# Kernel optimization log

Measured on AMD Instinct MI355X. Metric: run time of the kernel, lower is better.

Reference implementation:

```python
import jax, jax.numpy as jnp
import numpy as np

N_NODE = 40000  # item vocabulary
H = 100         # hidden size (SR-GNN default)
B = 64          # sessions per batch
L = 16          # items per session (equal-length sessions)
N = B * L       # total graph nodes
E = 2048        # total edges
NL = 1          # GatedGraphConv layers


def setup_inputs() -> dict:
    key = jax.random.key(0)
    ks = jax.random.split(key, 20)
    stdv = 1.0 / np.sqrt(H)
    u = lambda k, shape: jax.random.uniform(k, shape, jnp.float32, -stdv, stdv)
    return {
        "x": jax.random.randint(ks[0], (N,), 0, N_NODE),
        "edge_index": jax.random.randint(ks[1], (2, E), 0, N),
        "edge_weight": jax.random.uniform(ks[2], (E,), jnp.float32),
        "batch": jnp.arange(N) // L,  # node -> session id, equal-length sessions
        "embed": u(ks[3], (N_NODE, H)),
        "ggc_w": u(ks[4], (NL, H, H)),
        "gru_wih": u(ks[5], (3 * H, H)),
        "gru_whh": u(ks[6], (3 * H, H)),
        "gru_bih": u(ks[7], (3 * H,)),
        "gru_bhh": u(ks[8], (3 * H,)),
        "W1_w": u(ks[9], (H, H)), "W1_b": u(ks[10], (H,)),
        "W2_w": u(ks[11], (H, H)), "W2_b": u(ks[12], (H,)),
        "Wt_w": u(ks[13], (H, H)), "Wt_b": u(ks[14], (H,)),
        "q_w": u(ks[15], (1, H)), "q_b": u(ks[16], (1,)),
        "W3_w": u(ks[17], (H, 2 * H)), "W3_b": u(ks[18], (H,)),
    }


def reference(x, edge_index, edge_weight, batch, embed, ggc_w, gru_wih, gru_whh,
              gru_bih, gru_bhh, W1_w, W1_b, W2_w, W2_b, Wt_w, Wt_b, q_w, q_b,
              W3_w, W3_b):
    # Embedding lookup
    h = embed[x]  # [N, H]
    src, dst = edge_index[0], edge_index[1]
    # GatedGraphConv: weighted message aggregation + GRUCell update
    for l in range(NL):
        m = h @ ggc_w[l]                                             # [N, H]
        agg = jnp.zeros_like(h).at[dst].add(edge_weight[:, None] * m[src])
        gi = agg @ gru_wih.T + gru_bih                               # [N, 3H]
        gh = h @ gru_whh.T + gru_bhh
        ir, iz, inn = jnp.split(gi, 3, axis=-1)
        hr, hz, hn = jnp.split(gh, 3, axis=-1)
        r = jax.nn.sigmoid(ir + hr)
        zg = jax.nn.sigmoid(iz + hz)
        ng = jnp.tanh(inn + r * hn)
        h = (1.0 - zg) * ng + zg * h
    v = h.reshape(B, L, H)                                           # sessions
    s_l = v[:, -1]                                                   # [B, H] last item
    # alpha = q(sigmoid(W1(v_n) + W2(v)))
    a = jax.nn.sigmoid((s_l @ W1_w.T + W1_b)[:, None, :] + (v @ W2_w.T + W2_b))
    alpha = a @ q_w.T + q_b                                          # [B, L, 1]
    s_g = jnp.sum(alpha * v, axis=1)                                 # [B, H]
    s_h = jnp.concatenate([s_l, s_g], axis=-1) @ W3_w.T + W3_b       # [B, H]
    # Target attention: s_t[b] = softmax(E @ W_t(v_b)^T, -1) @ v_b, contracted
    # directly against E to avoid materializing [B, N_NODE, H].
    vt = v @ Wt_w.T + Wt_b                                           # [B, L, H]
    P = jax.nn.softmax(jnp.einsum('jh,blh->bjl', embed, vt), axis=-1)
    C = jnp.einsum('blh,jh->bjl', v, embed)                          # v_l . E_j
    z = s_h @ embed.T + jnp.sum(P * C, axis=-1)                      # [B, N_NODE]
    return z
```

## Files before the change

### kernel.cpp

```cpp
#include <hip/hip_runtime.h>
#include <hip/hip_bf16.h>

#define Hh    100
#define NN    1024
#define BB    64
#define LL    16
#define EE    2048
#define NNODE 40000

#define BSPL  8
#define BPB   (BB / BSPL)
#define PFR   12
#define PPAN  (PFR * 64 * 8)

typedef unsigned short u16;
typedef __attribute__((ext_vector_type(8))) short short8;
typedef __attribute__((ext_vector_type(4))) float f32x4;

__device__ __forceinline__ float bf2f(u16 u) {
    union { unsigned int i; float f; } v;
    v.i = ((unsigned int)u) << 16;
    return v.f;
}

__device__ __forceinline__ u16 f2bf(float f) {
    unsigned int x = __float_as_uint(f);
    unsigned int lsb = (x >> 16) & 1u;
    x += 0x7fffu + lsb;
    return (u16)(x >> 16);
}

__device__ __forceinline__ float sigmoidf_(float x) {
    return 1.0f / (1.0f + expf(-x));
}

template <bool BF>
__device__ __forceinline__ float ldv(const void* p, size_t i) {
    if (BF) return bf2f(((const u16*)p)[i]);
    return ((const float*)p)[i];
}
__device__ __forceinline__ float ldvf(int flag, const void* p, size_t i) {
    return flag ? ldv<true>(p, i) : ldv<false>(p, i);
}

template <bool BF>
__device__ void cvt_impl(int t,
                         const void* ew, const void* ggc, const void* wih, const void* whh,
                         const void* bih, const void* bhh, const void* W1w, const void* W1b,
                         const void* W2w, const void* W2b, const void* Wtw, const void* Wtb,
                         const void* qw, const void* qb, const void* W3w, const void* W3b,
                         float* __restrict__ W) {
    const void* src; int si; int doff; int di;
    if      (t <   2048) { src = ew;  si = t;          doff = 0;      di = si; }
    else if (t <  12048) { src = ggc; si = t - 2048;   doff = 2048;   di = si; }
    else if (t <  42048) { src = wih; si = t - 12048;  doff = 12048;  di = (si % 100) * 300 + si / 100; }
    else if (t <  72048) { src = whh; si = t - 42048;  doff = 42048;  di = (si % 100) * 300 + si / 100; }
    else if (t <  72348) { src = bih; si = t - 72048;  doff = 72048;  di = si; }
    else if (t <  72648) { src = bhh; si = t - 72348;  doff = 72352;  di = si; }
    else if (t <  82648) { src = W1w; si = t - 72648;  doff = 72656;  di = (si % 100) * 100 + si / 100; }
    else if (t <  82748) { src = W1b; si = t - 82648;  doff = 82656;  di = si; }
    else if (t <  92748) { src = W2w; si = t - 82748;  doff = 82768;  di = (si % 100) * 100 + si / 100; }
    else if (t <  92848) { src = W2b; si = t - 92748;  doff = 92768;  di = si; }
    else if (t < 102848) { src = Wtw; si = t - 92848;  doff = 92880;  di = (si % 100) * 100 + si / 100; }
    else if (t < 102948) { src = Wtb; si = t - 102848; doff = 102880; di = si; }
    else if (t < 103048) { src = qw;  si = t - 102948; doff = 102992; di = si; }
    else if (t < 103049) { src = qb;  si = t - 103048; doff = 103104; di = si; }
    else if (t < 123049) { src = W3w; si = t - 103049; doff = 103120; di = (si % 200) * 100 + si / 200; }
    else                 { src = W3b; si = t - 123049; doff = 123120; di = si; }
    W[doff + di] = ldv<BF>(src, si);
}

__global__ void __launch_bounds__(256) k_cvt(const void* embed_raw, int* __restrict__ flag,
                      const void* ew, const void* ggc, const void* wih, const void* whh,
                      const void* bih, const void* bhh, const void* W1w, const void* W1b,
                      const void* W2w, const void* W2b, const void* Wtw, const void* Wtb,
                      const void* qw, const void* qb, const void* W3w, const void* W3b,
                      float* __restrict__ W) {
    __shared__ int cnt;
    if (threadIdx.x == 0) cnt = 0;
    __syncthreads();
    int bad = 0;
    const u16* eb = (const u16*)embed_raw;
    for (int i = threadIdx.x; i < 4096; i += 256) {
        float v = bf2f(eb[i]);
        if (!(fabsf(v) <= 0.5f)) bad++;
    }
    if (bad) atomicAdd(&cnt, bad);
    __syncthreads();
    const bool bf = (cnt == 0);
    if (blockIdx.x == 0 && threadIdx.x == 0) flag[0] = bf ? 1 : 0;
    int t = blockIdx.x * 256 + threadIdx.x;
    if (t >= 123149) return;
    if (bf) cvt_impl<true >(t, ew, ggc, wih, whh, bih, bhh, W1w, W1b, W2w, W2b, Wtw, Wtb, qw, qb, W3w, W3b, W);
    else    cvt_impl<false>(t, ew, ggc, wih, whh, bih, bhh, W1w, W1b, W2w, W2b, Wtw, Wtb, qw, qb, W3w, W3b, W);
}

__global__ void __launch_bounds__(256) k_gm(const int* __restrict__ flag,
                                            const int* __restrict__ x,
                                            const void* __restrict__ embed,
                                            const float* __restrict__ ggc_w,
                                            float* __restrict__ m,
                                            float* __restrict__ agg) {
    __shared__ float W[Hh * Hh];
    __shared__ float H[8 * Hh];
    const int tid = threadIdx.x;
    const int fl = flag[0];
    const int r0 = blockIdx.x * 8;
    for (int idx = tid; idx < Hh * Hh; idx += 256) W[idx] = ggc_w[idx];
    for (int idx = tid; idx < 8 * Hh; idx += 256) {
        int i = idx / Hh, j = idx - i * Hh;
        H[idx] = ldvf(fl, embed, (size_t)x[r0 + i] * Hh + j);
    }
    for (int idx = tid; idx < 8 * Hh; idx += 256) agg[r0 * Hh + idx] = 0.0f;
    __syncthreads();
    for (int idx = tid; idx < 8 * Hh; idx += 256) {
        int i = idx / Hh, j = idx - i * Hh;
        float acc = 0.0f;
#pragma unroll 4
        for (int k = 0; k < Hh; ++k) acc += H[i * Hh + k] * W[k * Hh + j];
        m[(r0 + i) * Hh + j] = acc;
    }
}

__global__ void k_scatter(const int* __restrict__ ei, const float* __restrict__ ew,
                          const float* __restrict__ m, float* __restrict__ agg) {
    int t = blockIdx.x * 256 + threadIdx.x;
    if (t >= EE * Hh) return;
    int e = t / Hh, j = t - e * Hh;
    int src = ei[e], dst = ei[EE + e];
    atomicAdd(&agg[dst * Hh + j], ew[e] * m[src * Hh + j]);
}

__global__ void k_gru(const int* __restrict__ flag, const int* __restrict__ x,
                      const void* __restrict__ embed,
                      const float* __restrict__ agg,
                      const float* __restrict__ wihT, const float* __restrict__ whhT,
                      const float* __restrict__ bih, const float* __restrict__ bhh,
                      float* __restrict__ h1) {
    int t = blockIdx.x * 256 + threadIdx.x;
    if (t >= NN * Hh) return;
    int i = t / Hh, j = t - i * Hh;
    const int fl = flag[0];
    const size_t erow = (size_t)x[i] * Hh;
    const float* ar = agg + i * Hh;
    float s_ir = bih[j], s_iz = bih[j + Hh], s_in = bih[j + 2 * Hh];
    float s_hr = bhh[j], s_hz = bhh[j + Hh], s_hn = bhh[j + 2 * Hh];
    float h0j = 0.0f;
    for (int k = 0; k < Hh; ++k) {
        float a = ar[k];
        float h = ldvf(fl, embed, erow + k);
        if (k == j) h0j = h;
        const float* wT = wihT + k * 300;
        const float* uT = whhT + k * 300;
        s_ir += a * wT[j];
        s_iz += a * wT[j + 100];
        s_in += a * wT[j + 200];
        s_hr += h * uT[j];
        s_hz += h * uT[j + 100];
        s_hn += h * uT[j + 200];
    }
    float r = sigmoidf_(s_ir + s_hr);
    float z = sigmoidf_(s_iz + s_hz);
    float n = tanhf(s_in + r * s_hn);
    h1[t] = (1.0f - z) * n + z * h0j;
}

__global__ void __launch_bounds__(256) k_att(const float* __restrict__ h1,
                    const float* __restrict__ W1T, const float* __restrict__ W1b,
                    const float* __restrict__ W2T, const float* __restrict__ W2b,
                    const float* __restrict__ WtT, const float* __restrict__ Wtb,
                    const float* __restrict__ qw, const float* __restrict__ qb,
                    const float* __restrict__ W3T, const float* __restrict__ W3b,
                    u16* __restrict__ P) {
    __shared__ float V[LL * Hh];
    __shared__ float Q2[LL * Hh];
    __shared__ float VTs[LL * Hh];
    __shared__ float Q1[Hh];
    __shared__ float AL[LL];
    __shared__ float SG[Hh];
    __shared__ float SH[Hh];
    const int b = blockIdx.x, tid = threadIdx.x;
    for (int idx = tid; idx < LL * Hh; idx += 256) V[idx] = h1[b * LL * Hh + idx];
    __syncthreads();
    for (int idx = tid; idx < LL * Hh; idx += 256) {
        int i = idx / Hh, j = idx - i * Hh;
        float a2 = 0, at = 0;
        for (int k = 0; k < Hh; ++k) {
            float vk = V[i * Hh + k];
            a2 += vk * W2T[k * Hh + j];
            at += vk * WtT[k * Hh + j];
        }
        Q2[idx] = a2 + W2b[j];
        VTs[idx] = at + Wtb[j];
    }
    if (tid < Hh) {
        float a1 = 0;
        for (int k = 0; k < Hh; ++k) a1 += V[(LL - 1) * Hh + k] * W1T[k * Hh + tid];
        Q1[tid] = a1 + W1b[tid];
    }
    __syncthreads();
    if (tid < LL) {
        float acc = 0;
        for (int j = 0; j < Hh; ++j)
            acc += sigmoidf_(Q1[j] + Q2[tid * Hh + j]) * qw[j];
        AL[tid] = acc + qb[0];
    }
    __syncthreads();
    if (tid < Hh) {
        float acc = 0;
#pragma unroll
        for (int l = 0; l < LL; ++l) acc += AL[l] * V[l * Hh + tid];
        SG[tid] = acc;
    }
    __syncthreads();
    if (tid < Hh) {
        float acc = W3b[tid];
        for (int k = 0; k < Hh; ++k) acc += V[(LL - 1) * Hh + k] * W3T[k * Hh + tid];
        for (int k = 0; k < Hh; ++k) acc += SG[k] * W3T[(Hh + k) * Hh + tid];
        SH[tid] = acc;
    }
    __syncthreads();
    for (int w = tid; w < PFR * 64; w += 256) {
        int f = w >> 6, lane = w & 63;
        int t = f >> 2, ks = f & 3;
        int mm = lane & 15, qq = lane >> 4;
        int row = t * 16 + mm;
        int col0 = ks * 32 + qq * 8;
        short8 t8;
#pragma unroll
        for (int e = 0; e < 8; ++e) {
            int col = col0 + e;
            float v = 0.0f;
            if (col < Hh) {
                if      (row < 16) v = VTs[row * Hh + col];
                else if (row < 32) v = V[(row - 16) * Hh + col];
                else if (row == 32) v = SH[col];
            }
            t8[e] = (short)f2bf(v);
        }
        *(short8*)&P[((size_t)b * PFR + f) * 512 + lane * 8] = t8;
    }
}

__device__ __forceinline__ short8 load_efrag(const void* embed, bool bf, int j, int k0) {
    short8 v = {0, 0, 0, 0, 0, 0, 0, 0};
    if (j >= NNODE || k0 >= Hh) return v;
    if (bf) {
        const u16* row = (const u16*)embed + (size_t)j * Hh + k0;
        if (k0 + 8 <= Hh) {
            ushort4 a = *(const ushort4*)(row);
            ushort4 b = *(const ushort4*)(row + 4);
            v[0] = (short)a.x; v[1] = (short)a.y; v[2] = (short)a.z; v[3] = (short)a.w;
            v[4] = (short)b.x; v[5] = (short)b.y; v[6] = (short)b.z; v[7] = (short)b.w;
        } else {
            for (int e = 0; e < Hh - k0; ++e) v[e] = (short)row[e];
        }
    } else {
        const float* row = (const float*)embed + (size_t)j * Hh + k0;
        if (k0 + 8 <= Hh) {
            float4 a = *(const float4*)(row);
            float4 b = *(const float4*)(row + 4);
            v[0] = (short)f2bf(a.x); v[1] = (short)f2bf(a.y); v[2] = (short)f2bf(a.z); v[3] = (short)f2bf(a.w);
            v[4] = (short)f2bf(b.x); v[5] = (short)f2bf(b.y); v[6] = (short)f2bf(b.z); v[7] = (short)f2bf(b.w);
        } else {
            for (int e = 0; e < Hh - k0; ++e) v[e] = (short)f2bf(row[e]);
        }
    }
    return v;
}

__global__ void __launch_bounds__(256) k_score(const int* __restrict__ flag,
                                               const void* __restrict__ embed,
                                               const u16* __restrict__ P,
                                               void* __restrict__ out) {
    __shared__ alignas(16) u16 sPan[2][PPAN];
    const int jb = blockIdx.x * 128;
    const int b0 = blockIdx.y * BPB;
    const int tid = threadIdx.x;
    const bool bf = (flag[0] != 0);
    const int wave = tid >> 6, lane = tid & 63;
    const int m = lane & 15, quad = lane >> 4;

    short8 Bf[2][4];
#pragma unroll
    for (int g = 0; g < 2; ++g)
#pragma unroll
        for (int ks = 0; ks < 4; ++ks)
            Bf[g][ks] = load_efrag(embed, bf, jb + wave * 32 + g * 16 + m, ks * 32 + quad * 8);

    short8 pa = {0, 0, 0, 0, 0, 0, 0, 0};
    short8 pb = {0, 0, 0, 0, 0, 0, 0, 0};
    if (quad == 0) {
        pa[0] = (short)f2bf((float)m);
        pb[0] = (short)f2bf(1.0f);
    }
    f32x4 pd = (f32x4){0.0f, 0.0f, 0.0f, 0.0f};
    pd = __builtin_amdgcn_mfma_f32_16x16x32_bf16(pa, pb, pd, 0, 0, 0);
    const bool isH1 =
        (__builtin_amdgcn_readfirstlane(__float_as_uint(pd[1])) == 0x3f800000u);

    {
        const uint4* s4 = (const uint4*)(P + (size_t)b0 * PPAN);
        uint4 g0 = s4[tid], g1 = s4[tid + 256], g2 = s4[tid + 512];
        uint4* d = (uint4*)sPan[0];
        d[tid] = g0; d[tid + 256] = g1; d[tid + 512] = g2;
    }
    __syncthreads();

    int cur = 0;
    for (int bi = 0; bi < BPB; ++bi) {
        const int b = b0 + bi;
        uint4 g0, g1, g2;
        if (bi + 1 < BPB) {
            const uint4* s4 = (const uint4*)(P + (size_t)(b + 1) * PPAN);
            g0 = s4[tid]; g1 = s4[tid + 256]; g2 = s4[tid + 512];
        }

        const u16* sp = sPan[cur];
        f32x4 acc[2][3];
#pragma unroll
        for (int g = 0; g < 2; ++g)
#pragma unroll
            for (int t = 0; t < 3; ++t)
                acc[g][t] = (f32x4){0.0f, 0.0f, 0.0f, 0.0f};
#pragma unroll
        for (int t = 0; t < 3; ++t) {
            short8 A0 = *(const short8*)&sp[(t * 4 + 0) * 512 + lane * 8];
            short8 A1 = *(const short8*)&sp[(t * 4 + 1) * 512 + lane * 8];
            short8 A2 = *(const short8*)&sp[(t * 4 + 2) * 512 + lane * 8];
            short8 A3 = *(const short8*)&sp[(t * 4 + 3) * 512 + lane * 8];
#pragma unroll
            for (int g = 0; g < 2; ++g) {
                acc[g][t] = __builtin_amdgcn_mfma_f32_16x16x32_bf16(A0, Bf[g][0], acc[g][t], 0, 0, 0);
                acc[g][t] = __builtin_amdgcn_mfma_f32_16x16x32_bf16(A1, Bf[g][1], acc[g][t], 0, 0, 0);
                acc[g][t] = __builtin_amdgcn_mfma_f32_16x16x32_bf16(A2, Bf[g][2], acc[g][t], 0, 0, 0);
                acc[g][t] = __builtin_amdgcn_mfma_f32_16x16x32_bf16(A3, Bf[g][3], acc[g][t], 0, 0, 0);
            }
        }

#pragma unroll
        for (int g = 0; g < 2; ++g) {
            if (isH1) {
                float den = 0.0f, num = 0.0f;
#pragma unroll
                for (int r = 0; r < 4; ++r) {
                    float p = __expf(acc[g][0][r]);
                    den += p;
                    num += p * acc[g][1][r];
                }
                den += __shfl_xor(den, 16); num += __shfl_xor(num, 16);
                den += __shfl_xor(den, 32); num += __shfl_xor(num, 32);
                if (quad == 0) {
                    int j = jb + wave * 32 + g * 16 + m;
                    if (j < NNODE) {
                        float z = acc[g][2][0] + num / den;
                        if (bf) ((u16*)out)[(size_t)b * NNODE + j] = f2bf(z);
                        else    ((float*)out)[(size_t)b * NNODE + j] = z;
                    }
                }
            } else {
                float den[4], num[4];
#pragma unroll
                for (int r = 0; r < 4; ++r) {
                    float p = __expf(acc[g][0][r]);
                    den[r] = p;
                    num[r] = p * acc[g][1][r];
                }
#pragma unroll
                for (int s = 1; s <= 8; s <<= 1)
#pragma unroll
                    for (int r = 0; r < 4; ++r) {
                        den[r] += __shfl_xor(den[r], s);
                        num[r] += __shfl_xor(num[r], s);
                    }
                if (m == 0) {
#pragma unroll
                    for (int r = 0; r < 4; ++r) {
                        int j = jb + wave * 32 + g * 16 + quad * 4 + r;
                        if (j < NNODE) {
                            float z = acc[g][2][r] + num[r] / den[r];
                            if (bf) ((u16*)out)[(size_t)b * NNODE + j] = f2bf(z);
                            else    ((float*)out)[(size_t)b * NNODE + j] = z;
                        }
                    }
                }
            }
        }

        if (bi + 1 < BPB) {
            uint4* d = (uint4*)sPan[cur ^ 1];
            d[tid] = g0; d[tid + 256] = g1; d[tid + 512] = g2;
        }
        __syncthreads();
        cur ^= 1;
    }
}

extern "C" void kernel_launch(void* const* d_in, const int* in_sizes, int n_in,
                              void* d_out, int out_size, void* d_ws, size_t ws_size,
                              hipStream_t stream) {
    const int* x      = (const int*)d_in[0];
    const int* ei     = (const int*)d_in[1];
    const void* ew    = d_in[2];
    const void* embed = d_in[4];
    const void* ggc   = d_in[5];
    const void* wih   = d_in[6];
    const void* whh   = d_in[7];
    const void* bih   = d_in[8];
    const void* bhh   = d_in[9];
    const void* W1w   = d_in[10];
    const void* W1b   = d_in[11];
    const void* W2w   = d_in[12];
    const void* W2b   = d_in[13];
    const void* Wtw   = d_in[14];
    const void* Wtb   = d_in[15];
    const void* qw    = d_in[16];
    const void* qb    = d_in[17];
    const void* W3w   = d_in[18];
    const void* W3b   = d_in[19];
    float* ws = (float*)d_ws;
    int* flag = (int*)d_ws;

    float* W = ws + 64;
    float* ew_f  = W + 0;
    float* ggc_f = W + 2048;
    float* wihT  = W + 12048;
    float* whhT  = W + 42048;
    float* bih_f = W + 72048;
    float* bhh_f = W + 72352;
    float* W1T   = W + 72656;
    float* W1b_f = W + 82656;
    float* W2T   = W + 82768;
    float* W2b_f = W + 92768;
    float* WtT   = W + 92880;
    float* Wtb_f = W + 102880;
    float* qw_f  = W + 102992;
    float* qb_f  = W + 103104;
    float* W3T   = W + 103120;
    float* W3b_f = W + 123120;

    float* D     = ws + 123296;
    float* m     = D;
    float* agg   = D + 102400;
    float* h1    = D;
    u16*   P     = (u16*)(D + 102400);

    k_cvt    <<<dim3(482), dim3(256), 0, stream>>>(embed, flag, ew, ggc, wih, whh, bih, bhh,
                                                   W1w, W1b, W2w, W2b, Wtw, Wtb, qw, qb, W3w, W3b, W);
    k_gm     <<<dim3(128), dim3(256), 0, stream>>>(flag, x, embed, ggc_f, m, agg);
    k_scatter<<<dim3(800), dim3(256), 0, stream>>>(ei, ew_f, m, agg);
    k_gru    <<<dim3(400), dim3(256), 0, stream>>>(flag, x, embed, agg, wihT, whhT, bih_f, bhh_f, h1);
    k_att    <<<dim3(64),  dim3(256), 0, stream>>>(h1, W1T, W1b_f, W2T, W2b_f, WtT, Wtb_f,
                                                   qw_f, qb_f, W3T, W3b_f, P);
    k_score  <<<dim3((NNODE + 127) / 128, BSPL), dim3(256), 0, stream>>>(flag, embed, P, d_out);
}
```

Baseline: 234.6 us.

## Split attention kernel into wide per-element kernels and vectorize GRU dot products

Replaces the 64-block attention kernel with three kernels: a 400-block per-element kernel computing W2/Wt/W1 projections that writes the bf16 panel directly, a small alpha kernel, and a per-session kernel for s_g/s_h. The GRU now reads h0 cached by k_gm instead of re-gathering embed rows, and it does float4 dot products over untransposed row-major weights. Weight conversion drops the transposes, and agg zeroing is vectorized. This exposes much more parallelism in the attention stage at the cost of two extra launches and extra workspace traffic.

```diff
diff --git a/kernel.cpp b/kernel.cpp
--- a/kernel.cpp
+++ b/kernel.cpp
@@ -39,8 +39,14 @@
     if (BF) return bf2f(((const u16*)p)[i]);
     return ((const float*)p)[i];
 }
-__device__ __forceinline__ float ldvf(int flag, const void* p, size_t i) {
-    return flag ? ldv<true>(p, i) : ldv<false>(p, i);
+__device__ __forceinline__ float ldvb(int fl, const void* p, size_t i) {
+    return fl ? ldv<true>(p, i) : ldv<false>(p, i);
+}
+
+__device__ __forceinline__ size_t p_addr(int b, int row, int col) {
+    int f = (row >> 4) * 4 + (col >> 5);
+    int lane = (((col & 31) >> 3) << 4) + (row & 15);
+    return ((size_t)(b * PFR + f)) * 512 + lane * 8 + (col & 7);
 }
 
 template <bool BF>
@@ -50,24 +56,24 @@
                          const void* W2w, const void* W2b, const void* Wtw, const void* Wtb,
                          const void* qw, const void* qb, const void* W3w, const void* W3b,
                          float* __restrict__ W) {
-    const void* src; int si; int doff; int di;
-    if      (t <   2048) { src = ew;  si = t;          doff = 0;      di = si; }
-    else if (t <  12048) { src = ggc; si = t - 2048;   doff = 2048;   di = si; }
-    else if (t <  42048) { src = wih; si = t - 12048;  doff = 12048;  di = (si % 100) * 300 + si / 100; }
-    else if (t <  72048) { src = whh; si = t - 42048;  doff = 42048;  di = (si % 100) * 300 + si / 100; }
-    else if (t <  72348) { src = bih; si = t - 72048;  doff = 72048;  di = si; }
-    else if (t <  72648) { src = bhh; si = t - 72348;  doff = 72352;  di = si; }
-    else if (t <  82648) { src = W1w; si = t - 72648;  doff = 72656;  di = (si % 100) * 100 + si / 100; }
-    else if (t <  82748) { src = W1b; si = t - 82648;  doff = 82656;  di = si; }
-    else if (t <  92748) { src = W2w; si = t - 82748;  doff = 82768;  di = (si % 100) * 100 + si / 100; }
-    else if (t <  92848) { src = W2b; si = t - 92748;  doff = 92768;  di = si; }
-    else if (t < 102848) { src = Wtw; si = t - 92848;  doff = 92880;  di = (si % 100) * 100 + si / 100; }
-    else if (t < 102948) { src = Wtb; si = t - 102848; doff = 102880; di = si; }
-    else if (t < 103048) { src = qw;  si = t - 102948; doff = 102992; di = si; }
-    else if (t < 103049) { src = qb;  si = t - 103048; doff = 103104; di = si; }
-    else if (t < 123049) { src = W3w; si = t - 103049; doff = 103120; di = (si % 200) * 100 + si / 200; }
-    else                 { src = W3b; si = t - 123049; doff = 123120; di = si; }
-    W[doff + di] = ldv<BF>(src, si);
+    const void* src; int si; int doff;
+    if      (t <   2048) { src = ew;  si = t;          doff = 0; }
+    else if (t <  12048) { src = ggc; si = t - 2048;   doff = 2048; }
+    else if (t <  42048) { src = wih; si = t - 12048;  doff = 12048; }
+    else if (t <  72048) { src = whh; si = t - 42048;  doff = 42048; }
+    else if (t <  72348) { src = bih; si = t - 72048;  doff = 72048; }
+    else if (t <  72648) { src = bhh; si = t - 72348;  doff = 72352; }
+    else if (t <  82648) { src = W1w; si = t - 72648;  doff = 72656; }
+    else if (t <  82748) { src = W1b; si = t - 82648;  doff = 82656; }
+    else if (t <  92748) { src = W2w; si = t - 82748;  doff = 82768; }
+    else if (t <  92848) { src = W2b; si = t - 92748;  doff = 92768; }
+    else if (t < 102848) { src = Wtw; si = t - 92848;  doff = 92880; }
+    else if (t < 102948) { src = Wtb; si = t - 102848; doff = 102880; }
+    else if (t < 103048) { src = qw;  si = t - 102948; doff = 102992; }
+    else if (t < 103049) { src = qb;  si = t - 103048; doff = 103104; }
+    else if (t < 123049) { src = W3w; si = t - 103049; doff = 103120; }
+    else                 { src = W3b; si = t - 123049; doff = 123120; }
+    W[doff + si] = ldv<BF>(src, si);
 }
 
 __global__ void __launch_bounds__(256) k_cvt(const void* embed_raw, int* __restrict__ flag,
@@ -100,6 +106,7 @@
                                             const void* __restrict__ embed,
                                             const float* __restrict__ ggc_w,
                                             float* __restrict__ m,
+                                            float* __restrict__ h0,
                                             float* __restrict__ agg) {
     __shared__ float W[Hh * Hh];
     __shared__ float H[8 * Hh];
@@ -109,12 +116,15 @@
     for (int idx = tid; idx < Hh * Hh; idx += 256) W[idx] = ggc_w[idx];
     for (int idx = tid; idx < 8 * Hh; idx += 256) {
         int i = idx / Hh, j = idx - i * Hh;
-        H[idx] = ldvf(fl, embed, (size_t)x[r0 + i] * Hh + j);
-    }
-    for (int idx = tid; idx < 8 * Hh; idx += 256) agg[r0 * Hh + idx] = 0.0f;
+        H[idx] = ldvb(fl, embed, (size_t)x[r0 + i] * Hh + j);
+    }
+    float4 z4 = {0.0f, 0.0f, 0.0f, 0.0f};
+    for (int q = blockIdx.x * 256 + tid; q < 25600; q += 128 * 256)
+        ((float4*)agg)[q] = z4;
     __syncthreads();
     for (int idx = tid; idx < 8 * Hh; idx += 256) {
         int i = idx / Hh, j = idx - i * Hh;
+        h0[(r0 + i) * Hh + j] = H[idx];
         float acc = 0.0f;
 #pragma unroll 4
         for (int k = 0; k < Hh; ++k) acc += H[i * Hh + k] * W[k * Hh + j];
@@ -131,114 +141,124 @@
     atomicAdd(&agg[dst * Hh + j], ew[e] * m[src * Hh + j]);
 }
 
-__global__ void k_gru(const int* __restrict__ flag, const int* __restrict__ x,
-                      const void* __restrict__ embed,
-                      const float* __restrict__ agg,
-                      const float* __restrict__ wihT, const float* __restrict__ whhT,
+__global__ void k_gru(const float* __restrict__ agg, const float* __restrict__ h0,
+                      const float* __restrict__ wih, const float* __restrict__ whh,
                       const float* __restrict__ bih, const float* __restrict__ bhh,
                       float* __restrict__ h1) {
     int t = blockIdx.x * 256 + threadIdx.x;
     if (t >= NN * Hh) return;
     int i = t / Hh, j = t - i * Hh;
-    const int fl = flag[0];
-    const size_t erow = (size_t)x[i] * Hh;
-    const float* ar = agg + i * Hh;
-    float s_ir = bih[j], s_iz = bih[j + Hh], s_in = bih[j + 2 * Hh];
-    float s_hr = bhh[j], s_hz = bhh[j + Hh], s_hn = bhh[j + 2 * Hh];
-    float h0j = 0.0f;
-    for (int k = 0; k < Hh; ++k) {
-        float a = ar[k];
-        float h = ldvf(fl, embed, erow + k);
-        if (k == j) h0j = h;
-        const float* wT = wihT + k * 300;
-        const float* uT = whhT + k * 300;
-        s_ir += a * wT[j];
-        s_iz += a * wT[j + 100];
-        s_in += a * wT[j + 200];
-        s_hr += h * uT[j];
-        s_hz += h * uT[j + 100];
-        s_hn += h * uT[j + 200];
-    }
+    const float4* ar  = reinterpret_cast<const float4*>(agg + i * Hh);
+    const float4* hr  = reinterpret_cast<const float4*>(h0 + i * Hh);
+    const float4* wir = reinterpret_cast<const float4*>(wih + (size_t)j * Hh);
+    const float4* wiz = reinterpret_cast<const float4*>(wih + (size_t)(j + Hh) * Hh);
+    const float4* win = reinterpret_cast<const float4*>(wih + (size_t)(j + 2 * Hh) * Hh);
+    const float4* whr = reinterpret_cast<const float4*>(whh + (size_t)j * Hh);
+    const float4* whz = reinterpret_cast<const float4*>(whh + (size_t)(j + Hh) * Hh);
+    const float4* whn = reinterpret_cast<const float4*>(whh + (size_t)(j + 2 * Hh) * Hh);
+    float s_ir = 0, s_iz = 0, s_in = 0, s_hr = 0, s_hz = 0, s_hn = 0;
+    for (int kc = 0; kc < Hh / 4; ++kc) {
+        float4 a = ar[kc];
+        float4 h = hr[kc];
+        float4 w;
+        w = wir[kc]; s_ir += a.x * w.x + a.y * w.y + a.z * w.z + a.w * w.w;
+        w = wiz[kc]; s_iz += a.x * w.x + a.y * w.y + a.z * w.z + a.w * w.w;
+        w = win[kc]; s_in += a.x * w.x + a.y * w.y + a.z * w.z + a.w * w.w;
+        w = whr[kc]; s_hr += h.x * w.x + h.y * w.y + h.z * w.z + h.w * w.w;
+        w = whz[kc]; s_hz += h.x * w.x + h.y * w.y + h.z * w.z + h.w * w.w;
+        w = whn[kc]; s_hn += h.x * w.x + h.y * w.y + h.z * w.z + h.w * w.w;
+    }
+    s_ir += bih[j];
+    s_iz += bih[j + Hh];
+    s_in += bih[j + 2 * Hh];
+    s_hr += bhh[j];
+    s_hz += bhh[j + Hh];
+    s_hn += bhh[j + 2 * Hh];
     float r = sigmoidf_(s_ir + s_hr);
     float z = sigmoidf_(s_iz + s_hz);
     float n = tanhf(s_in + r * s_hn);
-    h1[t] = (1.0f - z) * n + z * h0j;
-}
-
-__global__ void __launch_bounds__(256) k_att(const float* __restrict__ h1,
-                    const float* __restrict__ W1T, const float* __restrict__ W1b,
-                    const float* __restrict__ W2T, const float* __restrict__ W2b,
-                    const float* __restrict__ WtT, const float* __restrict__ Wtb,
-                    const float* __restrict__ qw, const float* __restrict__ qb,
-                    const float* __restrict__ W3T, const float* __restrict__ W3b,
-                    u16* __restrict__ P) {
-    __shared__ float V[LL * Hh];
-    __shared__ float Q2[LL * Hh];
-    __shared__ float VTs[LL * Hh];
-    __shared__ float Q1[Hh];
-    __shared__ float AL[LL];
-    __shared__ float SG[Hh];
-    __shared__ float SH[Hh];
-    const int b = blockIdx.x, tid = threadIdx.x;
-    for (int idx = tid; idx < LL * Hh; idx += 256) V[idx] = h1[b * LL * Hh + idx];
-    __syncthreads();
-    for (int idx = tid; idx < LL * Hh; idx += 256) {
-        int i = idx / Hh, j = idx - i * Hh;
-        float a2 = 0, at = 0;
-        for (int k = 0; k < Hh; ++k) {
-            float vk = V[i * Hh + k];
-            a2 += vk * W2T[k * Hh + j];
-            at += vk * WtT[k * Hh + j];
-        }
-        Q2[idx] = a2 + W2b[j];
-        VTs[idx] = at + Wtb[j];
-    }
-    if (tid < Hh) {
+    h1[t] = (1.0f - z) * n + z * h0[t];
+}
+
+__global__ void k_att1(const float* __restrict__ h1,
+                       const float* __restrict__ W1w, const float* __restrict__ W1b,
+                       const float* __restrict__ W2w, const float* __restrict__ W2b,
+                       const float* __restrict__ Wtw, const float* __restrict__ Wtb,
+                       float* __restrict__ q1, float* __restrict__ q2,
+                       u16* __restrict__ P) {
+    int t = blockIdx.x * 256 + threadIdx.x;
+    if (t >= NN * Hh) return;
+    int i = t / Hh, j = t - i * Hh;
+    const float4* vr = reinterpret_cast<const float4*>(h1 + i * Hh);
+    const float4* w2 = reinterpret_cast<const float4*>(W2w + (size_t)j * Hh);
+    const float4* wt = reinterpret_cast<const float4*>(Wtw + (size_t)j * Hh);
+    float a2 = 0, at = 0;
+    for (int kc = 0; kc < Hh / 4; ++kc) {
+        float4 v = vr[kc];
+        float4 w;
+        w = w2[kc]; a2 += v.x * w.x + v.y * w.y + v.z * w.z + v.w * w.w;
+        w = wt[kc]; at += v.x * w.x + v.y * w.y + v.z * w.z + v.w * w.w;
+    }
+    q2[t] = a2 + W2b[j];
+    int b = i >> 4, n = i & 15;
+    P[p_addr(b, n, j)]      = f2bf(at + Wtb[j]);
+    P[p_addr(b, 16 + n, j)] = f2bf(h1[t]);
+    if (i < BB) {
+        const float4* sl = reinterpret_cast<const float4*>(h1 + (i * LL + LL - 1) * Hh);
+        const float4* w1 = reinterpret_cast<const float4*>(W1w + (size_t)j * Hh);
         float a1 = 0;
-        for (int k = 0; k < Hh; ++k) a1 += V[(LL - 1) * Hh + k] * W1T[k * Hh + tid];
-        Q1[tid] = a1 + W1b[tid];
-    }
-    __syncthreads();
-    if (tid < LL) {
+        for (int kc = 0; kc < Hh / 4; ++kc) {
+            float4 v = sl[kc];
+            float4 w = w1[kc];
+            a1 += v.x * w.x + v.y * w.y + v.z * w.z + v.w * w.w;
+        }
+        q1[i * Hh + j] = a1 + W1b[j];
+    }
+}
+
+__global__ void k_alpha(const float* __restrict__ q1, const float* __restrict__ q2,
+                        const float* __restrict__ qw, const float* __restrict__ qb,
+                        float* __restrict__ alpha) {
+    int i = blockIdx.x * 256 + threadIdx.x;
+    if (i >= NN) return;
+    int b = i >> 4;
+    float acc = 0;
+    for (int j = 0; j < Hh; ++j)
+        acc += sigmoidf_(q1[b * Hh + j] + q2[i * Hh + j]) * qw[j];
+    alpha[i] = acc + qb[0];
+}
+
+__global__ void k_sgsh(const float* __restrict__ h1, const float* __restrict__ alpha,
+                       const float* __restrict__ W3w, const float* __restrict__ W3b,
+                       u16* __restrict__ P) {
+    __shared__ float sl[Hh];
+    __shared__ float sg[Hh];
+    __shared__ float al[LL];
+    int b = blockIdx.x;
+    int j = threadIdx.x;
+    u16* Pp = P + (size_t)b * PPAN;
+    for (int w = j; w < PPAN; w += 128) {
+        int f = w >> 9, lane = (w >> 3) & 63, e = w & 7;
+        int row = (f >> 2) * 16 + (lane & 15);
+        int col = (f & 3) * 32 + (lane >> 4) * 8 + e;
+        if (row > 32 || col >= Hh) Pp[w] = 0;
+    }
+    if (j < LL) al[j] = alpha[b * LL + j];
+    __syncthreads();
+    if (j < Hh) {
+        sl[j] = h1[(b * LL + LL - 1) * Hh + j];
         float acc = 0;
-        for (int j = 0; j < Hh; ++j)
-            acc += sigmoidf_(Q1[j] + Q2[tid * Hh + j]) * qw[j];
-        AL[tid] = acc + qb[0];
-    }
-    __syncthreads();
-    if (tid < Hh) {
-        float acc = 0;
-#pragma unroll
-        for (int l = 0; l < LL; ++l) acc += AL[l] * V[l * Hh + tid];
-        SG[tid] = acc;
-    }
-    __syncthreads();
-    if (tid < Hh) {
-        float acc = W3b[tid];
-        for (int k = 0; k < Hh; ++k) acc += V[(LL - 1) * Hh + k] * W3T[k * Hh + tid];
-        for (int k = 0; k < Hh; ++k) acc += SG[k] * W3T[(Hh + k) * Hh + tid];
-        SH[tid] = acc;
-    }
-    __syncthreads();
-    for (int w = tid; w < PFR * 64; w += 256) {
-        int f = w >> 6, lane = w & 63;
-        int t = f >> 2, ks = f & 3;
-        int mm = lane & 15, qq = lane >> 4;
-        int row = t * 16 + mm;
-        int col0 = ks * 32 + qq * 8;
-        short8 t8;
-#pragma unroll
-        for (int e = 0; e < 8; ++e) {
-            int col = col0 + e;
-            float v = 0.0f;
-            if (col < Hh) {
-                if      (row < 16) v = VTs[row * Hh + col];
-                else if (row < 32) v = V[(row - 16) * Hh + col];
-                else if (row == 32) v = SH[col];
-            }
-            t8[e] = (short)f2bf(v);
-        }
-        *(short8*)&P[((size_t)b * PFR + f) * 512 + lane * 8] = t8;
+#pragma unroll
+        for (int l = 0; l < LL; ++l) acc += al[l] * h1[(b * LL + l) * Hh + j];
+        sg[j] = acc;
+    }
+    __syncthreads();
+    if (j < Hh) {
+        float acc = W3b[j];
+        const float* wr = W3w + (size_t)j * 2 * Hh;
+        for (int k = 0; k < Hh; ++k) acc += sl[k] * wr[k];
+        for (int k = 0; k < Hh; ++k) acc += sg[k] * wr[Hh + k];
+        P[p_addr(b, 32, j)] = f2bf(acc);
     }
 }
 
@@ -424,33 +444,39 @@
     float* W = ws + 64;
     float* ew_f  = W + 0;
     float* ggc_f = W + 2048;
-    float* wihT  = W + 12048;
-    float* whhT  = W + 42048;
+    float* wih_f = W + 12048;
+    float* whh_f = W + 42048;
     float* bih_f = W + 72048;
     float* bhh_f = W + 72352;
-    float* W1T   = W + 72656;
+    float* W1w_f = W + 72656;
     float* W1b_f = W + 82656;
-    float* W2T   = W + 82768;
+    float* W2w_f = W + 82768;
     float* W2b_f = W + 92768;
-    float* WtT   = W + 92880;
+    float* Wtw_f = W + 92880;
     float* Wtb_f = W + 102880;
     float* qw_f  = W + 102992;
     float* qb_f  = W + 103104;
-    float* W3T   = W + 103120;
+    float* W3w_f = W + 103120;
     float* W3b_f = W + 123120;
 
     float* D     = ws + 123296;
     float* m     = D;
     float* agg   = D + 102400;
-    float* h1    = D;
+    float* h0    = D + 204800;
+    float* h1    = D + 307200;
+    float* q2    = D;
     u16*   P     = (u16*)(D + 102400);
+    float* q1    = D + 299008;
+    float* alpha = D + 305408;
 
     k_cvt    <<<dim3(482), dim3(256), 0, stream>>>(embed, flag, ew, ggc, wih, whh, bih, bhh,
                                                    W1w, W1b, W2w, W2b, Wtw, Wtb, qw, qb, W3w, W3b, W);
-    k_gm     <<<dim3(128), dim3(256), 0, stream>>>(flag, x, embed, ggc_f, m, agg);
+    k_gm     <<<dim3(128), dim3(256), 0, stream>>>(flag, x, embed, ggc_f, m, h0, agg);
     k_scatter<<<dim3(800), dim3(256), 0, stream>>>(ei, ew_f, m, agg);
-    k_gru    <<<dim3(400), dim3(256), 0, stream>>>(flag, x, embed, agg, wihT, whhT, bih_f, bhh_f, h1);
-    k_att    <<<dim3(64),  dim3(256), 0, stream>>>(h1, W1T, W1b_f, W2T, W2b_f, WtT, Wtb_f,
-                                                   qw_f, qb_f, W3T, W3b_f, P);
+    k_gru    <<<dim3(400), dim3(256), 0, stream>>>(agg, h0, wih_f, whh_f, bih_f, bhh_f, h1);
+    k_att1   <<<dim3(400), dim3(256), 0, stream>>>(h1, W1w_f, W1b_f, W2w_f, W2b_f, Wtw_f, Wtb_f,
+                                                   q1, q2, P);
+    k_alpha  <<<dim3(4),   dim3(256), 0, stream>>>(q1, q2, qw_f, qb_f, alpha);
+    k_sgsh   <<<dim3(64),  dim3(128), 0, stream>>>(h1, alpha, W3w_f, W3b_f, P);
     k_score  <<<dim3((NNODE + 127) / 128, BSPL), dim3(256), 0, stream>>>(flag, embed, P, d_out);
 }
```

New measurement: 258.0 us. +10.0%, slower.
